# Kernel optimization log

Hardware: AMD Instinct MI355X
Metric: run time of the kernel (lower is better)

Reference implementation:

```python
import jax, jax.numpy as jnp
import numpy as np

ANCHORS = np.array([[10.0, 13.0], [16.0, 30.0], [33.0, 23.0]], dtype=np.float32)
IMG_SIZE = 416.0
NUM_CLASSES = 80
IGNORE_THR = 0.5
LAMBDA_XY, LAMBDA_WH, LAMBDA_CONF, LAMBDA_CLS = 1.0, 1.0, 5.0, 1.0
EPS = 1e-12


def setup_inputs() -> dict:
    key = jax.random.key(0)
    k1, k2, k3 = jax.random.split(key, 3)
    bs, A, nc, H, W, T = 32, 3, NUM_CLASSES, 52, 52, 50
    inp = jax.random.normal(k1, (bs, A * (5 + nc), H, W), dtype=jnp.float32)
    cls = jax.random.randint(k2, (bs, T, 1), 0, nc).astype(jnp.float32)
    coords = jax.random.uniform(k3, (bs, T, 4), minval=0.02, maxval=0.98, dtype=jnp.float32)
    targets = jnp.concatenate([cls, coords], axis=-1)  # (class, cx, cy, w, h), normalized
    return {"input": inp, "targets": targets}


def _bce(p, t):
    # elementwise binary cross entropy, sum-reduced by caller; torch convention 0*log(0)=0
    return -(t * jnp.log(jnp.clip(p, EPS, 1.0)) + (1.0 - t) * jnp.log(jnp.clip(1.0 - p, EPS, 1.0)))


def reference(input, targets):
    bs, _, H, W = input.shape
    anchors_px = jnp.asarray(ANCHORS)              # [A,2] in image pixels
    A = anchors_px.shape[0]
    nc = NUM_CLASSES
    stride = IMG_SIZE / H                          # square grid assumed (as in source)
    anchors = anchors_px / stride                  # scaled anchors [A,2]

    pred = input.reshape(bs, A, 5 + nc, H, W).transpose(0, 1, 3, 4, 2)  # [bs,A,H,W,5+nc]
    x = jax.nn.sigmoid(pred[..., 0])
    y = jax.nn.sigmoid(pred[..., 1])
    w = pred[..., 2]
    h = pred[..., 3]
    conf = jax.nn.sigmoid(pred[..., 4])
    pred_cls = jax.nn.sigmoid(pred[..., 5:])

    grid_x = jnp.arange(W, dtype=jnp.float32)[None, None, None, :]
    grid_y = jnp.arange(H, dtype=jnp.float32)[None, None, :, None]
    aw = anchors[:, 0][None, :, None, None]
    ah = anchors[:, 1][None, :, None, None]
    # pred boxes are detached in the original (uses .data)
    px = jax.lax.stop_gradient(x) + grid_x
    py = jax.lax.stop_gradient(y) + grid_y
    pw = jnp.exp(jax.lax.stop_gradient(w)) * aw
    ph = jnp.exp(jax.lax.stop_gradient(h)) * ah

    # ---- vectorized get_target ----
    targets = jax.lax.stop_gradient(targets)
    T = targets.shape[1]
    valid = jnp.sum(targets, axis=-1) > 0          # [bs,T]
    gx = targets[..., 1] * W
    gy = targets[..., 2] * H
    gw = targets[..., 3] * W
    gh = targets[..., 4] * H
    gi = jnp.clip(gx.astype(jnp.int32), 0, W - 1)  # [bs,T]
    gj = jnp.clip(gy.astype(jnp.int32), 0, H - 1)

    # anchor matching: wh-IoU at a common center
    inter_a = jnp.minimum(gw[..., None], anchors[:, 0]) * jnp.minimum(gh[..., None], anchors[:, 1])
    union_a = (gw * gh)[..., None] + anchors[:, 0] * anchors[:, 1] - inter_a
    anch_iou = inter_a / (union_a + 1e-16)         # [bs,T,A]
    best_n = jnp.argmax(anch_iou, axis=-1)         # [bs,T]

    # gt vs all predicted boxes (center-format IoU): [bs,T,A,H,W]
    b1x1 = (gx - gw / 2)[:, :, None, None, None]
    b1x2 = (gx + gw / 2)[:, :, None, None, None]
    b1y1 = (gy - gh / 2)[:, :, None, None, None]
    b1y2 = (gy + gh / 2)[:, :, None, None, None]
    b2x1 = (px - pw / 2)[:, None]
    b2x2 = (px + pw / 2)[:, None]
    b2y1 = (py - ph / 2)[:, None]
    b2y2 = (py + ph / 2)[:, None]
    iw = jnp.clip(jnp.minimum(b1x2, b2x2) - jnp.maximum(b1x1, b2x1), 0.0)
    ih = jnp.clip(jnp.minimum(b1y2, b2y2) - jnp.maximum(b1y1, b2y1), 0.0)
    inter_p = iw * ih
    area1 = (gw * gh)[:, :, None, None, None]
    area2 = (pw * ph)[:, None]
    pred_iou = inter_p / (area1 + area2 - inter_p + 1e-16)  # [bs,T,A,H,W]

    ignore = jnp.any((pred_iou >= IGNORE_THR) & valid[:, :, None, None, None], axis=1)
    noobj_mask = jnp.where(ignore, 0.0, 1.0)       # [bs,A,H,W]

    # scatter targets into the best (anchor, cell) of each gt box; invalid rows dropped
    b_idx = jnp.broadcast_to(jnp.arange(bs)[:, None], (bs, T))
    t_idx = jnp.broadcast_to(jnp.arange(T)[None, :], (bs, T))
    gi_s = jnp.where(valid, gi, W).reshape(-1)     # out-of-range -> mode='drop'
    bf = b_idx.reshape(-1)
    nf = best_n.reshape(-1)
    jf = gj.reshape(-1)

    zeros4 = jnp.zeros((bs, A, H, W), dtype=jnp.float32)
    mask = zeros4.at[bf, nf, jf, gi_s].set(1.0, mode='drop')
    noobj_mask = noobj_mask.at[bf, nf, jf, gi_s].set(0.0, mode='drop')
    tx = zeros4.at[bf, nf, jf, gi_s].set((gx - gi.astype(jnp.float32)).reshape(-1), mode='drop')
    ty = zeros4.at[bf, nf, jf, gi_s].set((gy - gj.astype(jnp.float32)).reshape(-1), mode='drop')
    tw_val = jnp.log(gw / anchors[best_n, 0] + 1e-16)
    th_val = jnp.log(gh / anchors[best_n, 1] + 1e-16)
    tw = zeros4.at[bf, nf, jf, gi_s].set(tw_val.reshape(-1), mode='drop')
    th = zeros4.at[bf, nf, jf, gi_s].set(th_val.reshape(-1), mode='drop')
    tconf_val = pred_iou[b_idx, t_idx, best_n, gj, gi]  # [bs,T] (stored but unused by losses)
    tconf = zeros4.at[bf, nf, jf, gi_s].set(tconf_val.reshape(-1), mode='drop')
    cls_f = jnp.clip(targets[..., 0].astype(jnp.int32), 0, nc - 1).reshape(-1)
    tcls = jnp.zeros((bs, A, H, W, nc), dtype=jnp.float32).at[bf, nf, jf, gi_s, cls_f].set(1.0, mode='drop')

    n_obj = jnp.maximum(jnp.sum(valid.astype(jnp.float32)), 1.0)

    # ---- losses (sum-reduced, as nn.MSELoss/BCELoss(size_average=False)) ----
    loss_x = jnp.sum((x * mask - tx * mask) ** 2) / (2 * n_obj)
    loss_y = jnp.sum((y * mask - ty * mask) ** 2) / (2 * n_obj)
    loss_w = jnp.sum((w * mask - tw * mask) ** 2) / (2 * n_obj)
    loss_h = jnp.sum((h * mask - th * mask) ** 2) / (2 * n_obj)
    # bce(conf*mask, mask): zero where mask==0 (bce(0,0)=0), -log(conf) where mask==1
    loss_conf_obj = -jnp.sum(mask * jnp.log(jnp.clip(conf, EPS, 1.0)))
    # bce(conf*noobj, 0): -log(1-conf) where noobj==1, zero elsewhere
    loss_conf_noobj = -jnp.sum(noobj_mask * jnp.log(jnp.clip(1.0 - conf, EPS, 1.0)))
    loss_conf = loss_conf_obj / n_obj + 0.2 * loss_conf_noobj / n_obj
    loss_cls = jnp.sum(mask[..., None] * _bce(pred_cls, tcls)) / n_obj

    loss = (loss_x * LAMBDA_XY + loss_y * LAMBDA_XY + loss_w * LAMBDA_WH + loss_h * LAMBDA_WH
            + loss_conf * LAMBDA_CONF + loss_cls * LAMBDA_CLS)

    # global_step < 12800 branch (early anchor-prior loss), always applied here
    a_loss = (jnp.sum((x - 0.5) ** 2) + jnp.sum((y - 0.5) ** 2)
              + jnp.sum(w ** 2) + jnp.sum(h ** 2)) / (2 * n_obj)
    loss = loss + 0.1 * a_loss
    return loss
```

## Files before the change

kernel.cpp:

```cpp
#include <hip/hip_runtime.h>
#include <math.h>

#define BS 32
#define NA 3
#define NC 80
#define HH 52
#define WW 52
#define TPER 50
#define NTT (BS * TPER)
#define HW (HH * WW)
#define CPB (NA * HW)
#define CH (5 + NC)
#define CELLS_PER_BLK 1024
#define CBPB 8
#define NCELLBLK (BS * CBPB)
#define NBLK (NCELLBLK + NTT)

__device__ __forceinline__ float sigm(float v) { return 1.0f / (1.0f + expf(-v)); }

__device__ __forceinline__ float wave_red(float t) {
    #pragma unroll
    for (int off = 32; off > 0; off >>= 1) t += __shfl_down(t, off);
    return t;
}


__global__ __launch_bounds__(256) void k_main(const float* __restrict__ in,
                                              const float* __restrict__ tgt,
                                              float2* __restrict__ ws)
{
    __shared__ float4 sbox[TPER];
    __shared__ int scell[TPER], scls[TPER];
    __shared__ unsigned sbm[CELLS_PER_BLK / 32];
    __shared__ float wred[4];
    const int tid = threadIdx.x;
    const float aw[3] = {1.25f, 2.0f, 4.125f};
    const float ah[3] = {1.625f, 3.75f, 2.875f};

    if (blockIdx.x < NCELLBLK) {
        const int b  = blockIdx.x >> 3;
        const int lo = (blockIdx.x & 7) * CELLS_PER_BLK;
        if (tid < CELLS_PER_BLK / 32) sbm[tid] = 0u;
        int mycell = -1;
        if (tid < TPER) {
            const float* p = tgt + (size_t)(b * TPER + tid) * 5;
            float c0 = p[0], c1 = p[1], c2 = p[2], c3 = p[3], c4 = p[4];
            bool valid = (c0 + c1 + c2 + c3 + c4) > 0.0f;
            float gx = c1 * WW, gy = c2 * HH, gw = c3 * WW, gh = c4 * HH;
            int gi = (int)gx; gi = gi < 0 ? 0 : (gi > WW - 1 ? WW - 1 : gi);
            int gj = (int)gy; gj = gj < 0 ? 0 : (gj > HH - 1 ? HH - 1 : gj);
            int bn = 0; float best = -1.0f;
            for (int a = 0; a < 3; ++a) {
                float inter = fminf(gw, aw[a]) * fminf(gh, ah[a]);
                float uni = gw * gh + aw[a] * ah[a] - inter;
                float iou = inter / (uni + 1e-16f);
                if (iou > best) { best = iou; bn = a; }
            }
            if (valid) {
                sbox[tid] = make_float4(gx - 0.5f * gw, gx + 0.5f * gw,
                                        gy - 0.5f * gh, gy + 0.5f * gh);
                mycell = bn * HW + gj * WW + gi;
            } else {
                sbox[tid] = make_float4(1e30f, 1e30f, 1e30f, 1e30f);
            }
        }
        __syncthreads();
        if (mycell >= lo && mycell < lo + CELLS_PER_BLK)
            atomicOr(&sbm[(mycell - lo) >> 5], 1u << ((mycell - lo) & 31));
        __syncthreads();

        const int idx0 = lo + tid;
        float term = 0.0f;
        float P1[4], P2[4], Q1[4], Q2[4], A2[4], CF[4];
        bool ACT[4], IGN[4] = {false, false, false, false};
        #pragma unroll
        for (int k = 0; k < 4; ++k) {
            int idx = idx0 + k * 256;
            ACT[k] = idx < CPB;
            P1[k] = 0.0f; P2[k] = 0.0f; Q1[k] = 0.0f; Q2[k] = 0.0f;
            A2[k] = 1e30f; CF[k] = 0.5f;
            if (ACT[k]) {
                int a = idx / HW;
                int r = idx - a * HW;
                int yy = r / WW;
                int xx = r - yy * WW;
                const float* base = in + ((size_t)b * (NA * CH) + a * CH) * HW + r;
                float xr = base[0], yr = base[HW], wr = base[2 * HW],
                      hr = base[3 * HW], cr = base[4 * HW];
                float sx = sigm(xr), sy = sigm(yr);
                CF[k] = sigm(cr);
                float px = sx + (float)xx, py = sy + (float)yy;
                float pw = expf(wr) * aw[a], ph = expf(hr) * ah[a];
                P1[k] = px - 0.5f * pw; P2[k] = px + 0.5f * pw;
                Q1[k] = py - 0.5f * ph; Q2[k] = py + 0.5f * ph;
                A2[k] = pw * ph + 1e-16f;
                term += 0.05f * ((sx - 0.5f) * (sx - 0.5f) + (sy - 0.5f) * (sy - 0.5f)
                                 + wr * wr + hr * hr);
            }
        }
        for (int t = 0; t < TPER; ++t) {
            float4 bx = sbox[t];
            float ar = (bx.y - bx.x) * (bx.w - bx.z);
            #pragma unroll
            for (int k = 0; k < 4; ++k) {
                float iw = fmaxf(fminf(bx.y, P2[k]) - fmaxf(bx.x, P1[k]), 0.0f);
                float ih = fmaxf(fminf(bx.w, Q2[k]) - fmaxf(bx.z, Q1[k]), 0.0f);
                float inter = iw * ih;
                IGN[k] = IGN[k] || (3.0f * inter >= ar + A2[k]);
            }
        }
        #pragma unroll
        for (int k = 0; k < 4; ++k) {
            int d = tid + k * 256;
            bool ist = (sbm[d >> 5] >> (d & 31)) & 1u;
            if (ACT[k] && !IGN[k] && !ist)
                term += -logf(fmaxf(1.0f - CF[k], 1e-12f));
        }
        term = wave_red(term);
        if ((tid & 63) == 0) wred[tid >> 6] = term;
        __syncthreads();
        if (tid == 0)
            ws[blockIdx.x] = make_float2(wred[0] + wred[1] + wred[2] + wred[3], 0.0f);
    } else {
        const int i = blockIdx.x - NCELLBLK;
        const int b = i / TPER;
        const int t = i - b * TPER;
        if (tid < TPER) {
            const float* p = tgt + (size_t)(b * TPER + tid) * 5;
            float c0 = p[0], c1 = p[1], c2 = p[2], c3 = p[3], c4 = p[4];
            bool valid = (c0 + c1 + c2 + c3 + c4) > 0.0f;
            float gx = c1 * WW, gy = c2 * HH, gw = c3 * WW, gh = c4 * HH;
            int gi = (int)gx; gi = gi < 0 ? 0 : (gi > WW - 1 ? WW - 1 : gi);
            int gj = (int)gy; gj = gj < 0 ? 0 : (gj > HH - 1 ? HH - 1 : gj);
            int bn = 0; float best = -1.0f;
            for (int a = 0; a < 3; ++a) {
                float inter = fminf(gw, aw[a]) * fminf(gh, ah[a]);
                float uni = gw * gh + aw[a] * ah[a] - inter;
                float iou = inter / (uni + 1e-16f);
                if (iou > best) { best = iou; bn = a; }
            }
            scell[tid] = valid ? (bn * HW + gj * WW + gi) : -1;
            int cls = (int)c0; cls = cls < 0 ? 0 : (cls > NC - 1 ? NC - 1 : cls);
            scls[tid] = cls;
        }
        __syncthreads();
        const int cell = scell[t];
        int a = 0, r = 0;
        float v = 0.0f;
        if (cell >= 0) {
            a = cell / HW;
            r = cell - a * HW;
            const float* bp = in + ((size_t)b * (NA * CH) + a * CH) * HW + r;
            if (tid < 85) v = bp[(size_t)tid * HW];
        }
        const int lane = tid & 63;
        bool m = (lane < TPER) && (cell >= 0) && (scell[lane] == cell);
        unsigned long long mask = __ballot(m);
        bool owner = (cell >= 0) && ((mask >> (t + 1)) == 0ULL);
        if (!owner) {
            if (tid == 0) ws[blockIdx.x] = make_float2(0.0f, cell >= 0 ? 1.0f : 0.0f);
            return;
        }
        float term = 0.0f;
        if (tid < 5) {
            const float* p = tgt + (size_t)i * 5;
            if (tid == 0) {
                float gx = p[1] * WW; int gi = r - (r / WW) * WW;
                float d = sigm(v) - (gx - (float)gi); term = 0.5f * d * d;
            } else if (tid == 1) {
                float gy = p[2] * HH; int gj = r / WW;
                float d = sigm(v) - (gy - (float)gj); term = 0.5f * d * d;
            } else if (tid == 2) {
                float d = v - logf(p[3] * WW / aw[a] + 1e-16f); term = 0.5f * d * d;
            } else if (tid == 3) {
                float d = v - logf(p[4] * HH / ah[a] + 1e-16f); term = 0.5f * d * d;
            } else {
                term = -5.0f * logf(fmaxf(sigm(v), 1e-12f));
            }
        } else if (tid < 85) {
            int c = tid - 5;
            bool pos = false;
            unsigned long long mm = mask;
            while (mm) { int t2 = __ffsll(mm) - 1; mm &= mm - 1; pos = pos || (scls[t2] == c); }
            float p = sigm(v);
            term = pos ? -logf(fmaxf(p, 1e-12f)) : -logf(fmaxf(1.0f - p, 1e-12f));
        }
        term = wave_red(term);
        if ((tid & 63) == 0) wred[tid >> 6] = term;
        __syncthreads();
        if (tid == 0)
            ws[blockIdx.x] = make_float2(wred[0] + wred[1] + wred[2] + wred[3], 1.0f);
    }
}

__global__ __launch_bounds__(256) void k_final(const float2* __restrict__ ws,
                                               float* __restrict__ out)
{
    const int tid = threadIdx.x;
    const float4* w4 = (const float4*)ws;
    float s = 0.0f, nv = 0.0f;
    for (int i = tid; i < NBLK / 2; i += 256) {
        float4 v = w4[i];
        s += v.x + v.z;
        nv += v.y + v.w;
    }
    __shared__ float wr0[4], wr1[4];
    s = wave_red(s);
    nv = wave_red(nv);
    if ((tid & 63) == 0) { wr0[tid >> 6] = s; wr1[tid >> 6] = nv; }
    __syncthreads();
    if (tid == 0) {
        float S = wr0[0] + wr0[1] + wr0[2] + wr0[3];
        float N = wr1[0] + wr1[1] + wr1[2] + wr1[3];
        out[0] = S / fmaxf(N, 1.0f);
    }
}

extern "C" void kernel_launch(void* const* d_in, const int* in_sizes, int n_in,
                              void* d_out, int out_size, void* d_ws, size_t ws_size,
                              hipStream_t stream)
{
    const float* in = (const float*)d_in[0];
    const float* tgt = (const float*)d_in[1];
    float2* ws = (float2*)d_ws;

    k_main<<<NBLK, 256, 0, stream>>>(in, tgt, ws);
    k_final<<<1, 256, 0, stream>>>(ws, (float*)d_out);
}
```

Before: 21.33 us.

## Pack two targets per object block and use fast exp/log intrinsics

Object blocks now each handle two targets, one per half of the 256 threads, which halves the number of object blocks and makes use of threads that previously sat idle past 85. Both paths share a single reduction epilogue. expf, logf and division are replaced with the hardware exp2, log and rcp intrinsics, and the anchor-IoU argmax now compares by cross-multiplication instead of division. The IoU loop is also unrolled by two. Approximate transcendentals may shift the loss slightly, and NBLK changes, so k_final must still read an even number of entries (1056 is even).

Result: faster. 18.53 us (-13.1%).

```diff
diff --git a/kernel.cpp b/kernel.cpp
--- a/kernel.cpp
+++ b/kernel.cpp
@@ -14,9 +14,13 @@
 #define CELLS_PER_BLK 1024
 #define CBPB 8
 #define NCELLBLK (BS * CBPB)
-#define NBLK (NCELLBLK + NTT)
-
-__device__ __forceinline__ float sigm(float v) { return 1.0f / (1.0f + expf(-v)); }
+#define OBJ_PAIRS 25
+#define NOBJBLK (BS * OBJ_PAIRS)
+#define NBLK (NCELLBLK + NOBJBLK)
+
+__device__ __forceinline__ float fexp(float x) { return __builtin_amdgcn_exp2f(x * 1.4426950408889634f); }
+__device__ __forceinline__ float flog(float x) { return __builtin_amdgcn_logf(x) * 0.6931471805599453f; }
+__device__ __forceinline__ float sigm(float v) { return __builtin_amdgcn_rcpf(1.0f + fexp(-v)); }
 
 __device__ __forceinline__ float wave_red(float t) {
     #pragma unroll
@@ -36,6 +40,11 @@
     const int tid = threadIdx.x;
     const float aw[3] = {1.25f, 2.0f, 4.125f};
     const float ah[3] = {1.625f, 3.75f, 2.875f};
+    const float raw[3] = {0.8f, 0.5f, 0.24242424242424243f};
+    const float rah[3] = {0.6153846153846154f, 0.26666666666666666f, 0.34782608695652173f};
+
+    float term = 0.0f;
+    float flag = 0.0f;
 
     if (blockIdx.x < NCELLBLK) {
         const int b  = blockIdx.x >> 3;
@@ -49,12 +58,16 @@
             float gx = c1 * WW, gy = c2 * HH, gw = c3 * WW, gh = c4 * HH;
             int gi = (int)gx; gi = gi < 0 ? 0 : (gi > WW - 1 ? WW - 1 : gi);
             int gj = (int)gy; gj = gj < 0 ? 0 : (gj > HH - 1 ? HH - 1 : gj);
-            int bn = 0; float best = -1.0f;
-            for (int a = 0; a < 3; ++a) {
-                float inter = fminf(gw, aw[a]) * fminf(gh, ah[a]);
-                float uni = gw * gh + aw[a] * ah[a] - inter;
-                float iou = inter / (uni + 1e-16f);
-                if (iou > best) { best = iou; bn = a; }
+            int bn = 0;
+            {
+                float bi = fminf(gw, aw[0]) * fminf(gh, ah[0]);
+                float bu = gw * gh + aw[0] * ah[0] - bi;
+                #pragma unroll
+                for (int a = 1; a < 3; ++a) {
+                    float ia = fminf(gw, aw[a]) * fminf(gh, ah[a]);
+                    float ua = gw * gh + aw[a] * ah[a] - ia;
+                    if (ia * bu > bi * ua) { bn = a; bi = ia; bu = ua; }
+                }
             }
             if (valid) {
                 sbox[tid] = make_float4(gx - 0.5f * gw, gx + 0.5f * gw,
@@ -70,7 +83,6 @@
         __syncthreads();
 
         const int idx0 = lo + tid;
-        float term = 0.0f;
         float P1[4], P2[4], Q1[4], Q2[4], A2[4], CF[4];
         bool ACT[4], IGN[4] = {false, false, false, false};
         #pragma unroll
@@ -90,7 +102,7 @@
                 float sx = sigm(xr), sy = sigm(yr);
                 CF[k] = sigm(cr);
                 float px = sx + (float)xx, py = sy + (float)yy;
-                float pw = expf(wr) * aw[a], ph = expf(hr) * ah[a];
+                float pw = fexp(wr) * aw[a], ph = fexp(hr) * ah[a];
                 P1[k] = px - 0.5f * pw; P2[k] = px + 0.5f * pw;
                 Q1[k] = py - 0.5f * ph; Q2[k] = py + 0.5f * ph;
                 A2[k] = pw * ph + 1e-16f;
@@ -98,6 +110,7 @@
                                  + wr * wr + hr * hr);
             }
         }
+        #pragma unroll 2
         for (int t = 0; t < TPER; ++t) {
             float4 bx = sbox[t];
             float ar = (bx.y - bx.x) * (bx.w - bx.z);
@@ -114,17 +127,13 @@
             int d = tid + k * 256;
             bool ist = (sbm[d >> 5] >> (d & 31)) & 1u;
             if (ACT[k] && !IGN[k] && !ist)
-                term += -logf(fmaxf(1.0f - CF[k], 1e-12f));
-        }
-        term = wave_red(term);
-        if ((tid & 63) == 0) wred[tid >> 6] = term;
-        __syncthreads();
-        if (tid == 0)
-            ws[blockIdx.x] = make_float2(wred[0] + wred[1] + wred[2] + wred[3], 0.0f);
+                term += -flog(fmaxf(1.0f - CF[k], 1e-12f));
+        }
     } else {
-        const int i = blockIdx.x - NCELLBLK;
-        const int b = i / TPER;
-        const int t = i - b * TPER;
+        const int o = blockIdx.x - NCELLBLK;
+        const int b = o / OBJ_PAIRS;
+        const int pair = o - b * OBJ_PAIRS;
+        const int tA = 2 * pair;
         if (tid < TPER) {
             const float* p = tgt + (size_t)(b * TPER + tid) * 5;
             float c0 = p[0], c1 = p[1], c2 = p[2], c3 = p[3], c4 = p[4];
@@ -132,65 +141,71 @@
             float gx = c1 * WW, gy = c2 * HH, gw = c3 * WW, gh = c4 * HH;
             int gi = (int)gx; gi = gi < 0 ? 0 : (gi > WW - 1 ? WW - 1 : gi);
             int gj = (int)gy; gj = gj < 0 ? 0 : (gj > HH - 1 ? HH - 1 : gj);
-            int bn = 0; float best = -1.0f;
-            for (int a = 0; a < 3; ++a) {
-                float inter = fminf(gw, aw[a]) * fminf(gh, ah[a]);
-                float uni = gw * gh + aw[a] * ah[a] - inter;
-                float iou = inter / (uni + 1e-16f);
-                if (iou > best) { best = iou; bn = a; }
+            int bn = 0;
+            {
+                float bi = fminf(gw, aw[0]) * fminf(gh, ah[0]);
+                float bu = gw * gh + aw[0] * ah[0] - bi;
+                #pragma unroll
+                for (int a = 1; a < 3; ++a) {
+                    float ia = fminf(gw, aw[a]) * fminf(gh, ah[a]);
+                    float ua = gw * gh + aw[a] * ah[a] - ia;
+                    if (ia * bu > bi * ua) { bn = a; bi = ia; bu = ua; }
+                }
             }
             scell[tid] = valid ? (bn * HW + gj * WW + gi) : -1;
             int cls = (int)c0; cls = cls < 0 ? 0 : (cls > NC - 1 ? NC - 1 : cls);
             scls[tid] = cls;
         }
         __syncthreads();
-        const int cell = scell[t];
+        const int half = tid >> 7;
+        const int myT = tA + half;
+        const int k = tid & 127;
+        const int cell = scell[myT];
         int a = 0, r = 0;
         float v = 0.0f;
-        if (cell >= 0) {
+        if (cell >= 0 && k < 85) {
             a = cell / HW;
             r = cell - a * HW;
-            const float* bp = in + ((size_t)b * (NA * CH) + a * CH) * HW + r;
-            if (tid < 85) v = bp[(size_t)tid * HW];
+            v = in[((size_t)b * (NA * CH) + a * CH + k) * HW + r];
         }
         const int lane = tid & 63;
         bool m = (lane < TPER) && (cell >= 0) && (scell[lane] == cell);
         unsigned long long mask = __ballot(m);
-        bool owner = (cell >= 0) && ((mask >> (t + 1)) == 0ULL);
-        if (!owner) {
-            if (tid == 0) ws[blockIdx.x] = make_float2(0.0f, cell >= 0 ? 1.0f : 0.0f);
-            return;
-        }
-        float term = 0.0f;
-        if (tid < 5) {
-            const float* p = tgt + (size_t)i * 5;
-            if (tid == 0) {
-                float gx = p[1] * WW; int gi = r - (r / WW) * WW;
-                float d = sigm(v) - (gx - (float)gi); term = 0.5f * d * d;
-            } else if (tid == 1) {
-                float gy = p[2] * HH; int gj = r / WW;
-                float d = sigm(v) - (gy - (float)gj); term = 0.5f * d * d;
-            } else if (tid == 2) {
-                float d = v - logf(p[3] * WW / aw[a] + 1e-16f); term = 0.5f * d * d;
-            } else if (tid == 3) {
-                float d = v - logf(p[4] * HH / ah[a] + 1e-16f); term = 0.5f * d * d;
-            } else {
-                term = -5.0f * logf(fmaxf(sigm(v), 1e-12f));
-            }
-        } else if (tid < 85) {
-            int c = tid - 5;
-            bool pos = false;
-            unsigned long long mm = mask;
-            while (mm) { int t2 = __ffsll(mm) - 1; mm &= mm - 1; pos = pos || (scls[t2] == c); }
-            float p = sigm(v);
-            term = pos ? -logf(fmaxf(p, 1e-12f)) : -logf(fmaxf(1.0f - p, 1e-12f));
-        }
-        term = wave_red(term);
-        if ((tid & 63) == 0) wred[tid >> 6] = term;
-        __syncthreads();
+        bool owner = (cell >= 0) && ((mask >> (myT + 1)) == 0ULL);
+        if (owner) {
+            if (k < 5) {
+                const float* p = tgt + (size_t)(b * TPER + myT) * 5;
+                if (k == 0) {
+                    float gx = p[1] * WW; int gi = r - (r / WW) * WW;
+                    float d = sigm(v) - (gx - (float)gi); term = 0.5f * d * d;
+                } else if (k == 1) {
+                    float gy = p[2] * HH; int gj = r / WW;
+                    float d = sigm(v) - (gy - (float)gj); term = 0.5f * d * d;
+                } else if (k == 2) {
+                    float d = v - flog(p[3] * WW * raw[a] + 1e-16f); term = 0.5f * d * d;
+                } else if (k == 3) {
+                    float d = v - flog(p[4] * HH * rah[a] + 1e-16f); term = 0.5f * d * d;
+                } else {
+                    term = -5.0f * flog(fmaxf(sigm(v), 1e-12f));
+                }
+            } else if (k < 85) {
+                int c = k - 5;
+                bool pos = false;
+                unsigned long long mm = mask;
+                while (mm) { int t2 = __ffsll(mm) - 1; mm &= mm - 1; pos = pos || (scls[t2] == c); }
+                float p = sigm(v);
+                term = pos ? -flog(fmaxf(p, 1e-12f)) : -flog(fmaxf(1.0f - p, 1e-12f));
+            }
+        }
         if (tid == 0)
-            ws[blockIdx.x] = make_float2(wred[0] + wred[1] + wred[2] + wred[3], 1.0f);
+            flag = (scell[tA] >= 0 ? 1.0f : 0.0f) + (scell[tA + 1] >= 0 ? 1.0f : 0.0f);
     }
+
+    float tr = wave_red(term);
+    if ((tid & 63) == 0) wred[tid >> 6] = tr;
+    __syncthreads();
+    if (tid == 0)
+        ws[blockIdx.x] = make_float2(wred[0] + wred[1] + wred[2] + wred[3], flag);
 }
 
 __global__ __launch_bounds__(256) void k_final(const float2* __restrict__ ws,
```
